# Kernel optimization log

Hardware: AMD Instinct MI355X
Metric: run time of the kernel (lower is better)

Reference implementation:

```python
import jax, jax.numpy as jnp
import numpy as np

N, F_IN, HEADS, D_HEAD, HID, OUT, E = 50000, 128, 4, 64, 256, 2, 800000
NEG_SLOPE = 0.2


def setup_inputs() -> dict:
    key = jax.random.key(0)
    ks = jax.random.split(key, 12)
    x = jax.random.normal(ks[0], (N, F_IN), dtype=jnp.float32)
    edge_index = jax.random.randint(ks[1], (2, E), 0, N, dtype=jnp.int64)
    s = 0.05
    W_gat = jax.random.normal(ks[2], (F_IN, HEADS * D_HEAD), dtype=jnp.float32) * s
    att_src = jax.random.normal(ks[3], (HEADS, D_HEAD), dtype=jnp.float32) * s
    att_dst = jax.random.normal(ks[4], (HEADS, D_HEAD), dtype=jnp.float32) * s
    b_gat = jnp.zeros((HEADS * D_HEAD,), dtype=jnp.float32)
    W1 = jax.random.normal(ks[5], (HEADS * D_HEAD, HID), dtype=jnp.float32) * s
    b1 = jnp.zeros((HID,), dtype=jnp.float32)
    W2 = jax.random.normal(ks[6], (HID, HID), dtype=jnp.float32) * s
    b2 = jnp.zeros((HID,), dtype=jnp.float32)
    W3 = jax.random.normal(ks[7], (HID, OUT), dtype=jnp.float32) * s
    b3 = jnp.zeros((OUT,), dtype=jnp.float32)
    return {"x": x, "edge_index": edge_index, "W_gat": W_gat, "att_src": att_src,
            "att_dst": att_dst, "b_gat": b_gat, "W1": W1, "b1": b1,
            "W2": W2, "b2": b2, "W3": W3, "b3": b3}


def _gat(x, edge_index, W_gat, att_src, att_dst, b_gat):
    n = x.shape[0]
    loop = jnp.arange(n, dtype=edge_index.dtype)
    src = jnp.concatenate([edge_index[0], loop])  # [E+N] message sources j
    dst = jnp.concatenate([edge_index[1], loop])  # [E+N] message targets i
    h = (x @ W_gat).reshape(n, HEADS, D_HEAD)      # [N,H,D]
    a_s = jnp.einsum('nhd,hd->nh', h, att_src)     # [N,H]
    a_d = jnp.einsum('nhd,hd->nh', h, att_dst)     # [N,H]
    e = a_s[src] + a_d[dst]                        # [E',H]
    e = jax.nn.leaky_relu(e, NEG_SLOPE)
    # per-destination-node softmax over incoming edges (numerically stable)
    emax = jax.ops.segment_max(e, dst, num_segments=n)
    e = jnp.exp(e - emax[dst])
    denom = jax.ops.segment_sum(e, dst, num_segments=n)
    alpha = e / denom[dst]                         # [E',H]
    msg = h[src] * alpha[:, :, None]               # [E',H,D]
    out = jax.ops.segment_sum(msg, dst, num_segments=n)  # [N,H,D]
    return out.reshape(n, HEADS * D_HEAD) + b_gat


def reference(x, edge_index, W_gat, att_src, att_dst, b_gat, W1, b1, W2, b2, W3, b3):
    h = _gat(x, edge_index, W_gat, att_src, att_dst, b_gat)
    h = jax.nn.relu(h @ W1 + b1)
    h = jax.nn.relu(h @ W2 + b2)
    return h @ W3 + b3
```

## Files before the change

### kernel.cpp

```cpp
#include <hip/hip_runtime.h>
#include <math.h>

#define N_NODES 50000
#define NP 50048
#define F_IN 128
#define HD 256
#define HID 256
#define NE 800000
#define CAP 64
#define NEG_SLOPE 0.2f

typedef __attribute__((ext_vector_type(8))) __bf16 bf16x8;
typedef __attribute__((ext_vector_type(4))) __bf16 bf16x4;
typedef __attribute__((ext_vector_type(4))) float f32x4;

#define GLD_LDS16(g, l)                                                      \
    __builtin_amdgcn_global_load_lds(                                        \
        (const __attribute__((address_space(1))) unsigned int*)(g),          \
        (__attribute__((address_space(3))) unsigned int*)(l), 16, 0, 0)

#define PB_INIT 196
#define PB_WG   128
#define PB_W1   256
#define PB_W2   256

__global__ __launch_bounds__(256) void prep_kernel(const float* __restrict__ Wg,
                                                   const float* __restrict__ W1,
                                                   const float* __restrict__ W2,
                                                   __bf16* __restrict__ Wg_t,
                                                   __bf16* __restrict__ W1_t,
                                                   __bf16* __restrict__ W2_t,
                                                   int* __restrict__ cnt,
                                                   unsigned short* __restrict__ bucket) {
    int b = blockIdx.x, t = threadIdx.x;
    if (b < PB_INIT) {
        int n = b * 256 + t;
        if (n < N_NODES) { cnt[n] = 1; bucket[n * CAP] = (unsigned short)n; }
    } else if (b < PB_INIT + PB_WG) {
        int i = (b - PB_INIT) * 256 + t;
        int m = i >> 7, k = i & 127;
        Wg_t[i] = (__bf16)Wg[(size_t)k * HD + m];
    } else if (b < PB_INIT + PB_WG + PB_W1) {
        int i = (b - PB_INIT - PB_WG) * 256 + t;
        int m = i >> 8, k = i & 255;
        W1_t[i] = (__bf16)W1[(size_t)k * HID + m];
    } else {
        int i = (b - PB_INIT - PB_WG - PB_W1) * 256 + t;
        int m = i >> 8, k = i & 255;
        W2_t[i] = (__bf16)W2[(size_t)k * HID + m];
    }
}

__global__ __launch_bounds__(256) void fill_kernel(const int* __restrict__ ew,
                                                   int* cnt,
                                                   unsigned short* __restrict__ bucket) {
    int e = blockIdx.x * 256 + threadIdx.x;
    int hi = ew[2 * e + 1];
    unsigned long long bal = __ballot(hi != 0);
    int src, dst;
    if (bal == 0) { src = ew[2 * e]; dst = ew[2 * NE + 2 * e]; }
    else          { src = ew[e];     dst = ew[NE + e]; }
    int pos = atomicAdd(&cnt[dst], 1);
    if (pos < CAP) bucket[dst * CAP + pos] = (unsigned short)src;
}

__global__ __launch_bounds__(256) void gemm1_attn_kernel(const float* __restrict__ x,
                                                         const __bf16* __restrict__ Bt,
                                                         const float* __restrict__ att_src,
                                                         const float* __restrict__ att_dst,
                                                         __bf16* __restrict__ h,
                                                         float* __restrict__ a_s,
                                                         float* __restrict__ a_d) {
    __shared__ __bf16 As[64 * 32];
    __shared__ __bf16 Bs[256 * 32];
    const int t = threadIdx.x;
    const int lane = t & 63, wv = t >> 6;
    const int lr = lane & 15, q = lane >> 4, lk = q * 8;
    const int col_off = wv * 64;
    const int row0 = blockIdx.x * 64;
    const int sr = t >> 2, sk = (t & 3) * 8;
    const int arow = row0 + sr;
    const bool avalid = arow < N_NODES;

    f32x4 acc[4][4];
#pragma unroll
    for (int r = 0; r < 4; ++r)
#pragma unroll
        for (int c = 0; c < 4; ++c) acc[r][c] = f32x4{0.f, 0.f, 0.f, 0.f};

    for (int k0 = 0; k0 < F_IN; k0 += 32) {
        float4 v0 = {0, 0, 0, 0}, v1 = {0, 0, 0, 0};
        if (avalid) {
            const float* xp = &x[(size_t)arow * F_IN + k0 + sk];
            v0 = *(const float4*)xp;
            v1 = *(const float4*)(xp + 4);
        }
        bf16x8 o;
        o[0] = (__bf16)v0.x; o[1] = (__bf16)v0.y; o[2] = (__bf16)v0.z; o[3] = (__bf16)v0.w;
        o[4] = (__bf16)v1.x; o[5] = (__bf16)v1.y; o[6] = (__bf16)v1.z; o[7] = (__bf16)v1.w;
        *(bf16x8*)&As[sr * 32 + sk] = o;
#pragma unroll
        for (int s = 0; s < 4; ++s) {
            int r = s * 64 + sr;
            GLD_LDS16(&Bt[(size_t)r * F_IN + k0 + sk], &Bs[r * 32 + sk]);
        }
        __syncthreads();
        bf16x8 af[4], bfr[4];
#pragma unroll
        for (int i = 0; i < 4; ++i) {
            af[i]  = *(const bf16x8*)&As[(i * 16 + lr) * 32 + lk];
            bfr[i] = *(const bf16x8*)&Bs[(col_off + i * 16 + lr) * 32 + lk];
        }
#pragma unroll
        for (int r = 0; r < 4; ++r)
#pragma unroll
            for (int c = 0; c < 4; ++c)
                acc[r][c] = __builtin_amdgcn_mfma_f32_16x16x32_bf16(af[r], bfr[c], acc[r][c], 0, 0, 0);
        __syncthreads();
    }

    float asv[4], adv[4];
#pragma unroll
    for (int c = 0; c < 4; ++c) {
        int col = col_off + c * 16 + lr;
        asv[c] = att_src[col];
        adv[c] = att_dst[col];
    }
    float ps[4][4], pd[4][4];
#pragma unroll
    for (int r = 0; r < 4; ++r)
#pragma unroll
        for (int i = 0; i < 4; ++i) { ps[r][i] = 0.f; pd[r][i] = 0.f; }

#pragma unroll
    for (int c = 0; c < 4; ++c) {
        int col = col_off + c * 16 + lr;
#pragma unroll
        for (int r = 0; r < 4; ++r) {
#pragma unroll
            for (int i = 0; i < 4; ++i) {
                int row = row0 + r * 16 + q * 4 + i;
                float v = acc[r][c][i];
                h[(size_t)row * HD + col] = (__bf16)v;
                ps[r][i] += v * asv[c];
                pd[r][i] += v * adv[c];
            }
        }
    }
#pragma unroll
    for (int r = 0; r < 4; ++r)
#pragma unroll
        for (int i = 0; i < 4; ++i) {
#pragma unroll
            for (int m = 1; m < 16; m <<= 1) {
                ps[r][i] += __shfl_xor(ps[r][i], m);
                pd[r][i] += __shfl_xor(pd[r][i], m);
            }
        }
    if (lr == 0) {
#pragma unroll
        for (int r = 0; r < 4; ++r)
#pragma unroll
            for (int i = 0; i < 4; ++i) {
                int row = row0 + r * 16 + q * 4 + i;
                a_s[row * 4 + wv] = ps[r][i];
                a_d[row * 4 + wv] = pd[r][i];
            }
    }
}

__device__ __forceinline__ float lrelu(float v) { return v >= 0.f ? v : NEG_SLOPE * v; }

__global__ __launch_bounds__(256) void gat_aggregate_kernel(const __bf16* __restrict__ h,
                                                            const float* __restrict__ a_s,
                                                            const float* __restrict__ a_d,
                                                            const int* __restrict__ cnt,
                                                            const unsigned short* __restrict__ bucket,
                                                            const float* __restrict__ b_gat,
                                                            __bf16* __restrict__ gat) {
    __shared__ unsigned short s_src[4][64];
    __shared__ float s_alpha[4][64][4];
    int lane = threadIdx.x & 63;
    int wv = threadIdx.x >> 6;
    int n = blockIdx.x * 4 + wv;

    int deg = cnt[n];
    if (deg > CAP) deg = CAP;
    int src = n;
    float4 e = {-1e30f, -1e30f, -1e30f, -1e30f};
    float4 ad = *(const float4*)&a_d[n * 4];
    if (lane < deg) {
        src = bucket[n * CAP + lane];
        float4 as4 = *(const float4*)&a_s[src * 4];
        e.x = lrelu(as4.x + ad.x);
        e.y = lrelu(as4.y + ad.y);
        e.z = lrelu(as4.z + ad.z);
        e.w = lrelu(as4.w + ad.w);
    }
    float4 m = e;
#pragma unroll
    for (int off = 1; off < 64; off <<= 1) {
        m.x = fmaxf(m.x, __shfl_xor(m.x, off));
        m.y = fmaxf(m.y, __shfl_xor(m.y, off));
        m.z = fmaxf(m.z, __shfl_xor(m.z, off));
        m.w = fmaxf(m.w, __shfl_xor(m.w, off));
    }
    float4 wgt = {0, 0, 0, 0};
    if (lane < deg) {
        wgt.x = __expf(e.x - m.x); wgt.y = __expf(e.y - m.y);
        wgt.z = __expf(e.z - m.z); wgt.w = __expf(e.w - m.w);
    }
    float4 s = wgt;
#pragma unroll
    for (int off = 1; off < 64; off <<= 1) {
        s.x += __shfl_xor(s.x, off); s.y += __shfl_xor(s.y, off);
        s.z += __shfl_xor(s.z, off); s.w += __shfl_xor(s.w, off);
    }
    s_src[wv][lane] = (unsigned short)src;
    s_alpha[wv][lane][0] = wgt.x / s.x;
    s_alpha[wv][lane][1] = wgt.y / s.y;
    s_alpha[wv][lane][2] = wgt.z / s.z;
    s_alpha[wv][lane][3] = wgt.w / s.w;
    __syncthreads();

    const int half = lane >> 5;
    const int l32 = lane & 31;
    const int c0 = l32 * 8;
    const int head = l32 >> 3;
    float acc[8];
#pragma unroll
    for (int k = 0; k < 8; ++k) acc[k] = 0.f;

    const int mde = (deg + 1) & ~1;
    int j = 0;
    for (; j + 4 <= mde; j += 4) {
        int j0 = j + half, j1 = j + 2 + half;
        int s0 = s_src[wv][j0], s1 = s_src[wv][j1];
        float a0 = s_alpha[wv][j0][head], a1 = s_alpha[wv][j1][head];
        bf16x8 h0 = *(const bf16x8*)&h[(size_t)s0 * HD + c0];
        bf16x8 h1 = *(const bf16x8*)&h[(size_t)s1 * HD + c0];
#pragma unroll
        for (int k = 0; k < 8; ++k)
            acc[k] += a0 * (float)h0[k] + a1 * (float)h1[k];
    }
    for (; j < mde; j += 2) {
        int j0 = j + half;
        int s0 = s_src[wv][j0];
        float a0 = s_alpha[wv][j0][head];
        bf16x8 h0 = *(const bf16x8*)&h[(size_t)s0 * HD + c0];
#pragma unroll
        for (int k = 0; k < 8; ++k)
            acc[k] += a0 * (float)h0[k];
    }
#pragma unroll
    for (int k = 0; k < 8; ++k) acc[k] += __shfl_xor(acc[k], 32);

    if (half == 0) {
        float4 bg0 = *(const float4*)&b_gat[c0];
        float4 bg1 = *(const float4*)&b_gat[c0 + 4];
        bf16x8 o;
        o[0] = (__bf16)(acc[0] + bg0.x); o[1] = (__bf16)(acc[1] + bg0.y);
        o[2] = (__bf16)(acc[2] + bg0.z); o[3] = (__bf16)(acc[3] + bg0.w);
        o[4] = (__bf16)(acc[4] + bg1.x); o[5] = (__bf16)(acc[5] + bg1.y);
        o[6] = (__bf16)(acc[6] + bg1.z); o[7] = (__bf16)(acc[7] + bg1.w);
        *(bf16x8*)&gat[(size_t)n * HD + c0] = o;
    }
}

__global__ __launch_bounds__(256) void fused_mlp_kernel(const __bf16* __restrict__ A,
                                                        const __bf16* __restrict__ W1t,
                                                        const __bf16* __restrict__ W2t,
                                                        const float* __restrict__ b1,
                                                        const float* __restrict__ b2,
                                                        const float* __restrict__ W3,
                                                        const float* __restrict__ b3,
                                                        float* __restrict__ out) {
    __shared__ __bf16 As[64 * 32];
    __shared__ __bf16 Ws[256 * 32];
    __shared__ __bf16 h1s[8 * 64 * 32];
    __shared__ float s_out[64][2];
    const int t = threadIdx.x;
    const int lane = t & 63, wv = t >> 6;
    const int lr = lane & 15, q = lane >> 4, lk = q * 8;
    const int col_off = wv * 64;
    const int row0 = blockIdx.x * 64;
    const int sr = t >> 2, sk = (t & 3) * 8;

    if (t < 128) ((float*)s_out)[t] = 0.f;

    f32x4 acc[4][4];
#pragma unroll
    for (int r = 0; r < 4; ++r)
#pragma unroll
        for (int c = 0; c < 4; ++c) acc[r][c] = f32x4{0.f, 0.f, 0.f, 0.f};

    for (int k0 = 0; k0 < HD; k0 += 32) {
        GLD_LDS16(&A[(size_t)(row0 + sr) * HD + k0 + sk], &As[sr * 32 + sk]);
#pragma unroll
        for (int s = 0; s < 4; ++s) {
            int r = s * 64 + sr;
            GLD_LDS16(&W1t[(size_t)r * HD + k0 + sk], &Ws[r * 32 + sk]);
        }
        __syncthreads();
        bf16x8 af[4], bfr[4];
#pragma unroll
        for (int i = 0; i < 4; ++i) {
            af[i]  = *(const bf16x8*)&As[(i * 16 + lr) * 32 + lk];
            bfr[i] = *(const bf16x8*)&Ws[(col_off + i * 16 + lr) * 32 + lk];
        }
#pragma unroll
        for (int r = 0; r < 4; ++r)
#pragma unroll
            for (int c = 0; c < 4; ++c)
                acc[r][c] = __builtin_amdgcn_mfma_f32_16x16x32_bf16(af[r], bfr[c], acc[r][c], 0, 0, 0);
        __syncthreads();
    }
#pragma unroll
    for (int c = 0; c < 4; ++c) {
        int col = col_off + c * 16 + lr;
        float bv = b1[col];
        int cb = (col >> 5) * 2048;
        int kk = col & 31;
#pragma unroll
        for (int r = 0; r < 4; ++r)
#pragma unroll
            for (int i = 0; i < 4; ++i) {
                int row = r * 16 + q * 4 + i;
                float v = fmaxf(acc[r][c][i] + bv, 0.f);
                h1s[cb + row * 32 + kk] = (__bf16)v;
                acc[r][c][i] = 0.f;
            }
    }
    __syncthreads();

    for (int k0 = 0; k0 < HID; k0 += 32) {
#pragma unroll
        for (int s = 0; s < 4; ++s) {
            int r = s * 64 + sr;
            GLD_LDS16(&W2t[(size_t)r * HID + k0 + sk], &Ws[r * 32 + sk]);
        }
        __syncthreads();
        const int cb = (k0 >> 5) * 2048;
        bf16x8 af[4], bfr[4];
#pragma unroll
        for (int i = 0; i < 4; ++i) {
            af[i]  = *(const bf16x8*)&h1s[cb + (i * 16 + lr) * 32 + lk];
            bfr[i] = *(const bf16x8*)&Ws[(col_off + i * 16 + lr) * 32 + lk];
        }
#pragma unroll
        for (int r = 0; r < 4; ++r)
#pragma unroll
            for (int c = 0; c < 4; ++c)
                acc[r][c] = __builtin_amdgcn_mfma_f32_16x16x32_bf16(af[r], bfr[c], acc[r][c], 0, 0, 0);
        __syncthreads();
    }

    float b2v[4], w30[4], w31[4];
#pragma unroll
    for (int c = 0; c < 4; ++c) {
        int col = col_off + c * 16 + lr;
        b2v[c] = b2[col];
        w30[c] = W3[col * 2];
        w31[c] = W3[col * 2 + 1];
    }
#pragma unroll
    for (int r = 0; r < 4; ++r) {
#pragma unroll
        for (int i = 0; i < 4; ++i) {
            float o0 = 0.f, o1 = 0.f;
#pragma unroll
            for (int c = 0; c < 4; ++c) {
                float v = fmaxf(acc[r][c][i] + b2v[c], 0.f);
                o0 += v * w30[c];
                o1 += v * w31[c];
            }
#pragma unroll
            for (int m = 1; m < 16; m <<= 1) {
                o0 += __shfl_xor(o0, m);
                o1 += __shfl_xor(o1, m);
            }
            if (lr == 0) {
                int row = r * 16 + q * 4 + i;
                atomicAdd(&s_out[row][0], o0);
                atomicAdd(&s_out[row][1], o1);
            }
        }
    }
    __syncthreads();
    if (t < 128) {
        int row = t >> 1, o = t & 1;
        int g = row0 + row;
        if (g < N_NODES) out[g * 2 + o] = s_out[row][o] + b3[o];
    }
}

extern "C" void kernel_launch(void* const* d_in, const int* in_sizes, int n_in,
                              void* d_out, int out_size, void* d_ws, size_t ws_size,
                              hipStream_t stream) {
    const float* x       = (const float*)d_in[0];
    const int*   ei      = (const int*)d_in[1];
    const float* W_gat   = (const float*)d_in[2];
    const float* att_src = (const float*)d_in[3];
    const float* att_dst = (const float*)d_in[4];
    const float* b_gat   = (const float*)d_in[5];
    const float* W1      = (const float*)d_in[6];
    const float* b1      = (const float*)d_in[7];
    const float* W2      = (const float*)d_in[8];
    const float* b2      = (const float*)d_in[9];
    const float* W3      = (const float*)d_in[10];
    const float* b3      = (const float*)d_in[11];
    float* out = (float*)d_out;

    char* ws = (char*)d_ws;
    __bf16* h_bf   = (__bf16*)ws;  ws += (size_t)NP * HD * 2;
    __bf16* gat_bf = (__bf16*)ws;  ws += (size_t)NP * HD * 2;
    __bf16* Wg_t   = (__bf16*)ws;  ws += (size_t)HD * F_IN * 2;
    __bf16* W1_t   = (__bf16*)ws;  ws += (size_t)HID * HD * 2;
    __bf16* W2_t   = (__bf16*)ws;  ws += (size_t)HID * HID * 2;
    float* a_s     = (float*)ws;   ws += (size_t)NP * 4 * 4;
    float* a_d     = (float*)ws;   ws += (size_t)NP * 4 * 4;
    int* cnt       = (int*)ws;     ws += (size_t)N_NODES * 4;
    unsigned short* bucket = (unsigned short*)ws;
    ws += (size_t)N_NODES * CAP * 2;

    prep_kernel<<<PB_INIT + PB_WG + PB_W1 + PB_W2, 256, 0, stream>>>(
        W_gat, W1, W2, Wg_t, W1_t, W2_t, cnt, bucket);
    fill_kernel<<<NE / 256, 256, 0, stream>>>(ei, cnt, bucket);
    gemm1_attn_kernel<<<NP / 64, 256, 0, stream>>>(x, Wg_t, att_src, att_dst,
                                                   h_bf, a_s, a_d);
    gat_aggregate_kernel<<<N_NODES / 4, 256, 0, stream>>>(h_bf, a_s, a_d, cnt, bucket,
                                                          b_gat, gat_bf);
    fused_mlp_kernel<<<NP / 64, 256, 0, stream>>>(gat_bf, W1_t, W2_t, b1, b2, W3, b3, out);
}
```

Measured before the change: 253.5 us.

## Fuse edge bucketing into GEMM1 launch, tile weight transposes, shrink aggregate blocks

Merges the edge-fill kernel and the first GEMM/attention kernel into one launch, with block ranges doing each job, so the two run concurrently and one launch disappears. GEMM1 tiles shrink from 64 to 32 rows and get an occupancy hint. Weight transposes go through a shared-memory tile for coalesced access. The aggregate kernel moves to 2-wave blocks, drops its block barrier (each wave reads only its own shared slice) and unrolls the gather loop to 4 neighbours per step. The risks are lower MFMA reuse per block and reliance on intra-wave ordering of shared-memory writes and reads now that the barrier is gone.

Result: no change. 254.2 us (+0.3%).

```diff
diff --git a/kernel.cpp b/kernel.cpp
--- a/kernel.cpp
+++ b/kernel.cpp
@@ -10,6 +10,9 @@
 #define CAP 64
 #define NEG_SLOPE 0.2f
 
+#define FILL_BLOCKS (NE / 256)
+#define G1_BLOCKS (NP / 32)
+
 typedef __attribute__((ext_vector_type(8))) __bf16 bf16x8;
 typedef __attribute__((ext_vector_type(4))) __bf16 bf16x4;
 typedef __attribute__((ext_vector_type(4))) float f32x4;
@@ -19,10 +22,33 @@
         (const __attribute__((address_space(1))) unsigned int*)(g),          \
         (__attribute__((address_space(3))) unsigned int*)(l), 16, 0, 0)
 
+__device__ __forceinline__ void tile_transpose(const float* __restrict__ W,
+                                               __bf16* __restrict__ Wt,
+                                               int K, int M, int k0, int m0, int t) {
+    __shared__ float tile[64][65];
+#pragma unroll
+    for (int i = 0; i < 4; ++i) {
+        int row = i * 16 + (t >> 4);
+        int col = (t & 15) * 4;
+        float4 v = *(const float4*)&W[(size_t)(k0 + row) * M + m0 + col];
+        tile[row][col] = v.x; tile[row][col + 1] = v.y;
+        tile[row][col + 2] = v.z; tile[row][col + 3] = v.w;
+    }
+    __syncthreads();
+#pragma unroll
+    for (int i = 0; i < 4; ++i) {
+        int mrow = i * 16 + (t >> 4);
+        int kcol = (t & 15) * 4;
+        bf16x4 o = {(__bf16)tile[kcol][mrow], (__bf16)tile[kcol + 1][mrow],
+                    (__bf16)tile[kcol + 2][mrow], (__bf16)tile[kcol + 3][mrow]};
+        *(bf16x4*)&Wt[(size_t)(m0 + mrow) * K + k0 + kcol] = o;
+    }
+}
+
 #define PB_INIT 196
-#define PB_WG   128
-#define PB_W1   256
-#define PB_W2   256
+#define PB_WG 8
+#define PB_W1 16
+#define PB_W2 16
 
 __global__ __launch_bounds__(256) void prep_kernel(const float* __restrict__ Wg,
                                                    const float* __restrict__ W1,
@@ -37,82 +63,78 @@
         int n = b * 256 + t;
         if (n < N_NODES) { cnt[n] = 1; bucket[n * CAP] = (unsigned short)n; }
     } else if (b < PB_INIT + PB_WG) {
-        int i = (b - PB_INIT) * 256 + t;
-        int m = i >> 7, k = i & 127;
-        Wg_t[i] = (__bf16)Wg[(size_t)k * HD + m];
+        int tt = b - PB_INIT;
+        tile_transpose(Wg, Wg_t, F_IN, HD, (tt >> 2) * 64, (tt & 3) * 64, t);
     } else if (b < PB_INIT + PB_WG + PB_W1) {
-        int i = (b - PB_INIT - PB_WG) * 256 + t;
-        int m = i >> 8, k = i & 255;
-        W1_t[i] = (__bf16)W1[(size_t)k * HID + m];
+        int tt = b - PB_INIT - PB_WG;
+        tile_transpose(W1, W1_t, HD, HID, (tt >> 2) * 64, (tt & 3) * 64, t);
     } else {
-        int i = (b - PB_INIT - PB_WG - PB_W1) * 256 + t;
-        int m = i >> 8, k = i & 255;
-        W2_t[i] = (__bf16)W2[(size_t)k * HID + m];
-    }
-}
-
-__global__ __launch_bounds__(256) void fill_kernel(const int* __restrict__ ew,
-                                                   int* cnt,
-                                                   unsigned short* __restrict__ bucket) {
-    int e = blockIdx.x * 256 + threadIdx.x;
-    int hi = ew[2 * e + 1];
-    unsigned long long bal = __ballot(hi != 0);
-    int src, dst;
-    if (bal == 0) { src = ew[2 * e]; dst = ew[2 * NE + 2 * e]; }
-    else          { src = ew[e];     dst = ew[NE + e]; }
-    int pos = atomicAdd(&cnt[dst], 1);
-    if (pos < CAP) bucket[dst * CAP + pos] = (unsigned short)src;
-}
-
-__global__ __launch_bounds__(256) void gemm1_attn_kernel(const float* __restrict__ x,
+        int tt = b - PB_INIT - PB_WG - PB_W1;
+        tile_transpose(W2, W2_t, HID, HID, (tt >> 2) * 64, (tt & 3) * 64, t);
+    }
+}
+
+__global__ __launch_bounds__(256, 6) void g1_fill_kernel(const float* __restrict__ x,
                                                          const __bf16* __restrict__ Bt,
                                                          const float* __restrict__ att_src,
                                                          const float* __restrict__ att_dst,
+                                                         const int* __restrict__ ew,
                                                          __bf16* __restrict__ h,
                                                          float* __restrict__ a_s,
-                                                         float* __restrict__ a_d) {
-    __shared__ __bf16 As[64 * 32];
+                                                         float* __restrict__ a_d,
+                                                         int* __restrict__ cnt,
+                                                         unsigned short* __restrict__ bucket) {
+    __shared__ __bf16 As[32 * 32];
     __shared__ __bf16 Bs[256 * 32];
+
+    if (blockIdx.x < FILL_BLOCKS) {
+        int e = blockIdx.x * 256 + threadIdx.x;
+        int hi = ew[2 * e + 1];
+        unsigned long long bal = __ballot(hi != 0);
+        int src, dst;
+        if (bal == 0) { src = ew[2 * e]; dst = ew[2 * NE + 2 * e]; }
+        else          { src = ew[e];     dst = ew[NE + e]; }
+        int pos = atomicAdd(&cnt[dst], 1);
+        if (pos < CAP) bucket[dst * CAP + pos] = (unsigned short)src;
+        return;
+    }
+
     const int t = threadIdx.x;
     const int lane = t & 63, wv = t >> 6;
     const int lr = lane & 15, q = lane >> 4, lk = q * 8;
     const int col_off = wv * 64;
-    const int row0 = blockIdx.x * 64;
-    const int sr = t >> 2, sk = (t & 3) * 8;
+    const int row0 = (blockIdx.x - FILL_BLOCKS) * 32;
+    const int sr = t >> 3, sk4 = (t & 7) * 4;
+    const int sb = t >> 2, skb = (t & 3) * 8;
     const int arow = row0 + sr;
     const bool avalid = arow < N_NODES;
 
-    f32x4 acc[4][4];
-#pragma unroll
-    for (int r = 0; r < 4; ++r)
+    f32x4 acc[2][4];
+#pragma unroll
+    for (int r = 0; r < 2; ++r)
 #pragma unroll
         for (int c = 0; c < 4; ++c) acc[r][c] = f32x4{0.f, 0.f, 0.f, 0.f};
 
     for (int k0 = 0; k0 < F_IN; k0 += 32) {
-        float4 v0 = {0, 0, 0, 0}, v1 = {0, 0, 0, 0};
-        if (avalid) {
-            const float* xp = &x[(size_t)arow * F_IN + k0 + sk];
-            v0 = *(const float4*)xp;
-            v1 = *(const float4*)(xp + 4);
-        }
-        bf16x8 o;
-        o[0] = (__bf16)v0.x; o[1] = (__bf16)v0.y; o[2] = (__bf16)v0.z; o[3] = (__bf16)v0.w;
-        o[4] = (__bf16)v1.x; o[5] = (__bf16)v1.y; o[6] = (__bf16)v1.z; o[7] = (__bf16)v1.w;
-        *(bf16x8*)&As[sr * 32 + sk] = o;
+        float4 v = {0, 0, 0, 0};
+        if (avalid) v = *(const float4*)&x[(size_t)arow * F_IN + k0 + sk4];
+        bf16x4 o = {(__bf16)v.x, (__bf16)v.y, (__bf16)v.z, (__bf16)v.w};
+        *(bf16x4*)&As[sr * 32 + sk4] = o;
 #pragma unroll
         for (int s = 0; s < 4; ++s) {
-            int r = s * 64 + sr;
-            GLD_LDS16(&Bt[(size_t)r * F_IN + k0 + sk], &Bs[r * 32 + sk]);
-        }
-        __syncthreads();
-        bf16x8 af[4], bfr[4];
-#pragma unroll
-        for (int i = 0; i < 4; ++i) {
-            af[i]  = *(const bf16x8*)&As[(i * 16 + lr) * 32 + lk];
-            bfr[i] = *(const bf16x8*)&Bs[(col_off + i * 16 + lr) * 32 + lk];
-        }
-#pragma unroll
-        for (int r = 0; r < 4; ++r)
+            int r = s * 64 + sb;
+            GLD_LDS16(&Bt[(size_t)r * F_IN + k0 + skb], &Bs[r * 32 + skb]);
+        }
+        __syncthreads();
+        bf16x8 af[2], bfr[4];
+#pragma unroll
+        for (int i = 0; i < 2; ++i)
+            af[i] = *(const bf16x8*)&As[(i * 16 + lr) * 32 + lk];
+#pragma unroll
+        for (int c = 0; c < 4; ++c)
+            bfr[c] = *(const bf16x8*)&Bs[(col_off + c * 16 + lr) * 32 + lk];
+#pragma unroll
+        for (int r = 0; r < 2; ++r)
 #pragma unroll
             for (int c = 0; c < 4; ++c)
                 acc[r][c] = __builtin_amdgcn_mfma_f32_16x16x32_bf16(af[r], bfr[c], acc[r][c], 0, 0, 0);
@@ -126,9 +148,9 @@
         asv[c] = att_src[col];
         adv[c] = att_dst[col];
     }
-    float ps[4][4], pd[4][4];
-#pragma unroll
-    for (int r = 0; r < 4; ++r)
+    float ps[2][4], pd[2][4];
+#pragma unroll
+    for (int r = 0; r < 2; ++r)
 #pragma unroll
         for (int i = 0; i < 4; ++i) { ps[r][i] = 0.f; pd[r][i] = 0.f; }
 
@@ -136,7 +158,7 @@
     for (int c = 0; c < 4; ++c) {
         int col = col_off + c * 16 + lr;
 #pragma unroll
-        for (int r = 0; r < 4; ++r) {
+        for (int r = 0; r < 2; ++r) {
 #pragma unroll
             for (int i = 0; i < 4; ++i) {
                 int row = row0 + r * 16 + q * 4 + i;
@@ -148,7 +170,7 @@
         }
     }
 #pragma unroll
-    for (int r = 0; r < 4; ++r)
+    for (int r = 0; r < 2; ++r)
 #pragma unroll
         for (int i = 0; i < 4; ++i) {
 #pragma unroll
@@ -159,7 +181,7 @@
         }
     if (lr == 0) {
 #pragma unroll
-        for (int r = 0; r < 4; ++r)
+        for (int r = 0; r < 2; ++r)
 #pragma unroll
             for (int i = 0; i < 4; ++i) {
                 int row = row0 + r * 16 + q * 4 + i;
@@ -171,18 +193,18 @@
 
 __device__ __forceinline__ float lrelu(float v) { return v >= 0.f ? v : NEG_SLOPE * v; }
 
-__global__ __launch_bounds__(256) void gat_aggregate_kernel(const __bf16* __restrict__ h,
+__global__ __launch_bounds__(128) void gat_aggregate_kernel(const __bf16* __restrict__ h,
                                                             const float* __restrict__ a_s,
                                                             const float* __restrict__ a_d,
                                                             const int* __restrict__ cnt,
                                                             const unsigned short* __restrict__ bucket,
                                                             const float* __restrict__ b_gat,
                                                             __bf16* __restrict__ gat) {
-    __shared__ unsigned short s_src[4][64];
-    __shared__ float s_alpha[4][64][4];
-    int lane = threadIdx.x & 63;
-    int wv = threadIdx.x >> 6;
-    int n = blockIdx.x * 4 + wv;
+    __shared__ unsigned short s_src[2][64];
+    __shared__ float s_alpha[2][64][4];
+    const int lane = threadIdx.x & 63;
+    const int wv = threadIdx.x >> 6;
+    const int n = blockIdx.x * 2 + wv;
 
     int deg = cnt[n];
     if (deg > CAP) deg = CAP;
@@ -221,7 +243,6 @@
     s_alpha[wv][lane][1] = wgt.y / s.y;
     s_alpha[wv][lane][2] = wgt.z / s.z;
     s_alpha[wv][lane][3] = wgt.w / s.w;
-    __syncthreads();
 
     const int half = lane >> 5;
     const int l32 = lane & 31;
@@ -233,15 +254,20 @@
 
     const int mde = (deg + 1) & ~1;
     int j = 0;
-    for (; j + 4 <= mde; j += 4) {
-        int j0 = j + half, j1 = j + 2 + half;
+    for (; j + 8 <= mde; j += 8) {
+        int j0 = j + half, j1 = j + 2 + half, j2 = j + 4 + half, j3 = j + 6 + half;
         int s0 = s_src[wv][j0], s1 = s_src[wv][j1];
+        int s2 = s_src[wv][j2], s3 = s_src[wv][j3];
         float a0 = s_alpha[wv][j0][head], a1 = s_alpha[wv][j1][head];
+        float a2 = s_alpha[wv][j2][head], a3 = s_alpha[wv][j3][head];
         bf16x8 h0 = *(const bf16x8*)&h[(size_t)s0 * HD + c0];
         bf16x8 h1 = *(const bf16x8*)&h[(size_t)s1 * HD + c0];
+        bf16x8 h2 = *(const bf16x8*)&h[(size_t)s2 * HD + c0];
+        bf16x8 h3 = *(const bf16x8*)&h[(size_t)s3 * HD + c0];
 #pragma unroll
         for (int k = 0; k < 8; ++k)
-            acc[k] += a0 * (float)h0[k] + a1 * (float)h1[k];
+            acc[k] += a0 * (float)h0[k] + a1 * (float)h1[k]
+                    + a2 * (float)h2[k] + a3 * (float)h3[k];
     }
     for (; j < mde; j += 2) {
         int j0 = j + half;
@@ -425,10 +451,9 @@
 
     prep_kernel<<<PB_INIT + PB_WG + PB_W1 + PB_W2, 256, 0, stream>>>(
         W_gat, W1, W2, Wg_t, W1_t, W2_t, cnt, bucket);
-    fill_kernel<<<NE / 256, 256, 0, stream>>>(ei, cnt, bucket);
-    gemm1_attn_kernel<<<NP / 64, 256, 0, stream>>>(x, Wg_t, att_src, att_dst,
-                                                   h_bf, a_s, a_d);
-    gat_aggregate_kernel<<<N_NODES / 4, 256, 0, stream>>>(h_bf, a_s, a_d, cnt, bucket,
+    g1_fill_kernel<<<FILL_BLOCKS + G1_BLOCKS, 256, 0, stream>>>(
+        x, Wg_t, att_src, att_dst, ei, h_bf, a_s, a_d, cnt, bucket);
+    gat_aggregate_kernel<<<N_NODES / 2, 128, 0, stream>>>(h_bf, a_s, a_d, cnt, bucket,
                                                           b_gat, gat_bf);
     fused_mlp_kernel<<<NP / 64, 256, 0, stream>>>(gat_bf, W1_t, W2_t, b1, b2, W3, b3, out);
 }
```
